# Kernel tuning notes

Hardware: AMD Instinct MI355X
Metric: run time of the kernel (lower is better)

The kernel has to match this reference:

```python
import jax, jax.numpy as jnp
import numpy as np

PAD_ID = 1
NEG = jnp.float32(-1e30)


def setup_inputs() -> dict:
    key = jax.random.key(0)
    ks = jax.random.split(key, 12)
    T, B, S, D, E, V = 20, 32, 400, 512, 512, 50000
    s = 0.02  # weight init scale for numerical sanity
    return {
        "inputs": jax.random.randint(ks[0], (T, B), 0, V),
        "src": jax.random.randint(ks[1], (S, B, 1), 0, V),
        "h_e": jax.random.normal(ks[2], (S, B, D), jnp.float32),
        "h0": jnp.zeros((B, D), jnp.float32),
        "c0": jnp.zeros((B, D), jnp.float32),
        "W_emb": jax.random.normal(ks[3], (V, E), jnp.float32) * s,
        "W_proj": jax.random.normal(ks[4], (E, 3 * D), jnp.float32) * s,
        "b_out": jax.random.normal(ks[5], (V,), jnp.float32) * s,
        "proj_u_W": jax.random.normal(ks[6], (1, 3 * D), jnp.float32) * s,
        "proj_u_b": jnp.zeros((1,), jnp.float32),
        "enc_W": jax.random.normal(ks[7], (D, D), jnp.float32) * s,
        "dec_W": jax.random.normal(ks[8], (D, D), jnp.float32) * s,
        "W_ih": jax.random.normal(ks[9], (4 * D, E), jnp.float32) * s,
        "W_hh": jax.random.normal(ks[10], (4 * D, D), jnp.float32) * s,
        "b_ih": jnp.zeros((4 * D,), jnp.float32),
        "b_hh": jnp.zeros((4 * D,), jnp.float32),
    }


def reference(inputs, src, h_e, h0, c0, W_emb, W_proj, b_out, proj_u_W,
              proj_u_b, enc_W, dec_W, W_ih, W_hh, b_ih, b_hh):
    T, B = inputs.shape
    D = h0.shape[1]
    V = W_emb.shape[0]
    src_bs = src[:, :, 0].T                       # [B, S]
    # Sect 2.4 shared output weights: W_out = tanh(W_emb @ W_proj)  [V, 3D]
    W_out = jnp.tanh(W_emb @ W_proj)
    rows = jnp.arange(B)[:, None]
    tpos = jnp.arange(T)

    def step(carry, xs):
        h, c, hist = carry                        # hist: [T, B, D] decoder-state history
        inp_t, t = xs
        emb = W_emb[inp_t]                        # [B, E]
        # single-layer LSTM cell (torch gate order i, f, g, o)
        gates = emb @ W_ih.T + h @ W_hh.T + b_ih + b_hh
        i, f, g, o = jnp.split(gates, 4, axis=-1)
        c_new = jax.nn.sigmoid(f) * c + jax.nn.sigmoid(i) * jnp.tanh(g)
        hd = jax.nn.sigmoid(o) * jnp.tanh(c_new)  # [B, D]
        # encoder intra-attention
        q = hd @ enc_W.T
        ae = jax.nn.softmax(jnp.einsum('bd,sbd->bs', q, h_e), axis=-1)  # [B, S]
        ce = jnp.einsum('bs,sbd->bd', ae, h_e)
        # decoder intra-attention over steps < t (zero context at t==0)
        qd = hd @ dec_W.T
        sd = jnp.einsum('bd,tbd->bt', qd, hist)
        sd = jnp.where(tpos[None, :] < t, sd, NEG)
        ad = jax.nn.softmax(sd, axis=-1)
        cd = jnp.where(t > 0, jnp.einsum('bt,tbd->bd', ad, hist), 0.0)
        hist = hist.at[t].set(hd)
        # pointer-generator
        ccat = jnp.concatenate([hd, ce, cd], axis=-1)        # [B, 3D]
        logits = ccat @ W_out.T + b_out                      # [B, V]
        logits = logits.at[:, PAD_ID].set(NEG)
        p_gen = jax.nn.softmax(logits, axis=-1)
        p_switch = jax.nn.sigmoid(ccat @ proj_u_W.T + proj_u_b)  # [B, 1]
        # copy distribution: scatter attention into vocab
        copy = jnp.zeros((B, V), logits.dtype).at[rows, src_bs].add(ae)
        scores = copy * p_switch + p_gen * (1.0 - p_switch)
        return (hd, c_new, hist), scores

    hist0 = jnp.zeros((T, B, D), h0.dtype)
    _, scores = jax.lax.scan(step, (h0, c0, hist0), (inputs, tpos))
    return scores  # [T, B, V]
```

## Files before the change

### kernel.cpp

```cpp
#include <hip/hip_runtime.h>
#include <stdint.h>

typedef unsigned short u16;
typedef unsigned int   u32;

using f32x4 = __attribute__((ext_vector_type(4))) float;
using s16x8 = __attribute__((ext_vector_type(8))) short;

#define TT 20
#define BB 32
#define SS 400
#define DD 512
#define VV 50000
#define VP 50048

__device__ __forceinline__ float bf2f(u16 u){
  u32 x = ((u32)u) << 16;
  return __builtin_bit_cast(float, x);
}
__device__ __forceinline__ u16 f2bf(float f){
  u32 x = __builtin_bit_cast(u32, f);
  x = x + 0x7fffu + ((x >> 16) & 1u);
  return (u16)(x >> 16);
}
__device__ __forceinline__ float sigm(float x){ return 1.0f/(1.0f + __expf(-x)); }
__device__ __forceinline__ float tanh_fast(float x){
  float a = fabsf(x);
  if (a < 0.25f){ float x2 = x*x; return x + x*x2*(-0.33333334f + 0.13333334f*x2); }
  return tanhf(x);
}
__device__ __forceinline__ void gld16(const void* g, void* l){
  __builtin_amdgcn_global_load_lds((const __attribute__((address_space(1))) void*)g,
                                   (__attribute__((address_space(3))) void*)l, 16, 0, 0);
}

__global__ __launch_bounds__(256) void k_prep(
    const float* __restrict__ W_proj,
    const float* __restrict__ W_ih,   const float* __restrict__ W_hh,
    const float* __restrict__ b_ih,   const float* __restrict__ b_hh,
    const float* __restrict__ h0,     const float* __restrict__ c0,
    const float* __restrict__ enc_W,  const float* __restrict__ dec_W,
    u16* __restrict__ WpT,
    u16* __restrict__ Wihs, u16* __restrict__ Whhs,
    u16* __restrict__ encWb, u16* __restrict__ decWb, float* __restrict__ bgs,
    float* __restrict__ hist, u16* __restrict__ histb, float* __restrict__ c_st,
    float* __restrict__ psE)
{
  int i = blockIdx.x*256 + threadIdx.x;
  if (i < 1280){ psE[i] = 0.0f; return; }
  i -= 1280;
  if (i < 2048){ int d = i >> 2, g = i & 3; bgs[i] = b_ih[g*512 + d] + b_hh[g*512 + d]; return; }
  i -= 2048;
  if (i < 16384){ float hv = h0[i]; hist[i] = hv; histb[i] = f2bf(hv); c_st[i] = c0[i]; return; }
  i -= 16384;
  if (i < 786432){ int j = i >> 9, k = i & 511; WpT[i] = f2bf(W_proj[k*1536 + j]); return; }
  i -= 786432;
  if (i < 1048576){
    int mp = i >> 9, k = i & 511; int d = mp >> 2, g = mp & 3;
    Wihs[i] = f2bf(W_ih[(size_t)(g*512 + d)*512 + k]); return; }
  i -= 1048576;
  if (i < 1048576){
    int mp = i >> 9, k = i & 511; int d = mp >> 2, g = mp & 3;
    Whhs[i] = f2bf(W_hh[(size_t)(g*512 + d)*512 + k]); return; }
  i -= 1048576;
  if (i < 262144){ encWb[i] = f2bf(enc_W[i]); return; }
  i -= 262144;
  if (i < 262144){ decWb[i] = f2bf(dec_W[i]); return; }
}

__global__ __launch_bounds__(256) void k_cast_emb(const float* __restrict__ in, u16* __restrict__ out){
  int i = blockIdx.x*256 + threadIdx.x;
  int base = i*4;
  if (base >= VP*DD) return;
  uint2 o;
  if (base < VV*DD){
    float4 v = *(const float4*)&in[base];
    o.x = (u32)f2bf(v.x) | ((u32)f2bf(v.y) << 16);
    o.y = (u32)f2bf(v.z) | ((u32)f2bf(v.w) << 16);
  } else { o.x = 0u; o.y = 0u; }
  *(uint2*)&out[base] = o;
}

__global__ __launch_bounds__(256) void k_cast_he(const float* __restrict__ in, u16* __restrict__ out){
  int i = blockIdx.x*256 + threadIdx.x;
  int base = i*4;
  if (base >= SS*BB*DD) return;
  const int s = base >> 14;
  const int b = (base >> 9) & 31;
  const int d = base & 511;
  float4 v = *(const float4*)&in[base];
  uint2 o;
  o.x = (u32)f2bf(v.x) | ((u32)f2bf(v.y) << 16);
  o.y = (u32)f2bf(v.z) | ((u32)f2bf(v.w) << 16);
  *(uint2*)&out[((size_t)(b*SS + s) << 9) + d] = o;
}

__global__ __launch_bounds__(256) void k_gather(const int* __restrict__ inp,
                                                const u16* __restrict__ Wb, u16* __restrict__ out){
  int i = blockIdx.x*256 + threadIdx.x;
  if (i >= TT*BB*DD) return;
  int r = i >> 9, k = i & 511;
  out[i] = Wb[(size_t)inp[r]*DD + k];
}

template<int EPI>
__device__ __forceinline__ void gemm_tile(
    const u16* __restrict__ A, const u16* __restrict__ B,
    float* __restrict__ Cf, u16* __restrict__ Cb, const float* __restrict__ bias,
    int K, int mt, int nt, int ldc, int nmax, char* smemc)
{
  u16* As = (u16*)smemc;
  u16* Bs = (u16*)(smemc + 8192);
  const int tid = threadIdx.x;
  const int w = tid >> 6, l = tid & 63;
  const int m0 = mt*128, n0 = nt*128;
  const int sgrow = l >> 2;
  const int sgk = (((l & 3) ^ ((l >> 3) & 3))) * 8;
  const int wm = (w >> 1)*64, wn = (w & 1)*64;
  const int fr = l & 15;
  const int fk = (((l >> 4) ^ ((l >> 1) & 3))) * 8;
  f32x4 acc[4][4] = {};
  for (int k0 = 0; k0 < K; k0 += 32){
    #pragma unroll
    for (int i = 0; i < 2; ++i){
      const int ci = w + i*4;
      gld16(A + (size_t)(m0 + ci*16 + sgrow)*K + (k0 + sgk), &As[ci*512]);
      gld16(B + (size_t)(n0 + ci*16 + sgrow)*K + (k0 + sgk), &Bs[ci*512]);
    }
    __syncthreads();
    s16x8 af[4], bfr[4];
    #pragma unroll
    for (int i = 0; i < 4; ++i){
      af[i]  = *(const s16x8*)&As[(wm + i*16 + fr)*32 + fk];
      bfr[i] = *(const s16x8*)&Bs[(wn + i*16 + fr)*32 + fk];
    }
    #pragma unroll
    for (int i = 0; i < 4; ++i)
      #pragma unroll
      for (int j = 0; j < 4; ++j)
        acc[i][j] = __builtin_amdgcn_mfma_f32_16x16x32_bf16(af[i], bfr[j], acc[i][j], 0, 0, 0);
    __syncthreads();
  }
  #pragma unroll
  for (int i = 0; i < 4; ++i){
    #pragma unroll
    for (int j = 0; j < 4; ++j){
      #pragma unroll
      for (int r = 0; r < 4; ++r){
        const int row = m0 + wm + i*16 + (l >> 4)*4 + r;
        const int col = n0 + wn + j*16 + fr;
        const float v = acc[i][j][r];
        if constexpr (EPI == 0){ Cf[(size_t)row*ldc + col] = v; }
        else if constexpr (EPI == 1){ Cb[(size_t)row*ldc + col] = f2bf(tanh_fast(v)); }
        else { if (col < nmax) Cb[(size_t)row*ldc + col] = f2bf(v + bias[col]); }
      }
    }
  }
}

template<int EPI, int ORD>
__global__ __launch_bounds__(256) void gemm_bt(
    const u16* __restrict__ A, const u16* __restrict__ B,
    float* __restrict__ Cf, u16* __restrict__ Cb, const float* __restrict__ bias,
    int K, int TM, int TN, int ldc, int nmax)
{
  __shared__ __align__(16) char smem[16384];
  int bid = blockIdx.x;
  if (ORD >= 1){
    const int n = TM*TN, x = bid & 7, i = bid >> 3;
    const int q = n >> 3, r = n & 7;
    bid = (x < r ? x*(q+1) : r*(q+1) + (x-r)*q) + i;
  }
  const int mt = (ORD == 1) ? bid / TN : bid % TM;
  const int nt = (ORD == 1) ? bid % TN : bid / TM;
  gemm_tile<EPI>(A, B, Cf, Cb, bias, K, mt, nt, ldc, nmax, smem);
}

__global__ __launch_bounds__(256) void k_lstm(
    const u16* __restrict__ Whhs, const float* __restrict__ X, const float* __restrict__ bgs,
    float* __restrict__ hist, u16* __restrict__ histb, float* __restrict__ c_st,
    u16* __restrict__ ccatb, int t)
{
  __shared__ __align__(16) u16 Hs[32*512];
  __shared__ __align__(16) u16 As[16*512];
  __shared__ float Cp[4][16][32];
  const int blk = blockIdx.x;
  const int tid = threadIdx.x;
  const int w = tid >> 6, l = tid & 63;
  const char* hsrc = (const char*)(histb + (size_t)t*16384);
  #pragma unroll
  for (int p = 0; p < 8; ++p)
    gld16(hsrc + p*4096 + w*1024 + l*16, (char*)Hs + p*4096 + w*1024);
  const char* asrc = (const char*)(Whhs + (size_t)blk*16*512);
  #pragma unroll
  for (int p = 0; p < 4; ++p)
    gld16(asrc + p*4096 + w*1024 + l*16, (char*)As + p*4096 + w*1024);
  __syncthreads();
  {
    const int fr = l & 15, fko = (l >> 4)*8;
    f32x4 acc0 = {}, acc1 = {};
    #pragma unroll
    for (int kk = 0; kk < 4; ++kk){
      const int kb = (w*4 + kk)*32;
      s16x8 af = *(const s16x8*)&As[fr*512 + kb + fko];
      s16x8 b0 = *(const s16x8*)&Hs[fr*512 + kb + fko];
      s16x8 b1 = *(const s16x8*)&Hs[(16 + fr)*512 + kb + fko];
      acc0 = __builtin_amdgcn_mfma_f32_16x16x32_bf16(af, b0, acc0, 0, 0, 0);
      acc1 = __builtin_amdgcn_mfma_f32_16x16x32_bf16(af, b1, acc1, 0, 0, 0);
    }
    #pragma unroll
    for (int r = 0; r < 4; ++r){
      Cp[w][(l >> 4)*4 + r][fr]      = acc0[r];
      Cp[w][(l >> 4)*4 + r][16 + fr] = acc1[r];
    }
  }
  __syncthreads();
  if (tid < 128){
    const int dl = tid >> 5, b = tid & 31;
    const int d = blk*4 + dl;
    const int bd = b*512 + d;
    float gv[4];
    #pragma unroll
    for (int g = 0; g < 4; ++g)
      gv[g] = Cp[0][dl*4 + g][b] + Cp[1][dl*4 + g][b] + Cp[2][dl*4 + g][b] + Cp[3][dl*4 + g][b];
    const float4 x4 = *(const float4*)&X[((size_t)(t*BB + b))*2048 + d*4];
    const float4 g4 = *(const float4*)&bgs[d*4];
    const float iv = gv[0] + x4.x + g4.x;
    const float fv = gv[1] + x4.y + g4.y;
    const float gg = gv[2] + x4.z + g4.z;
    const float ov = gv[3] + x4.w + g4.w;
    const float cn = sigm(fv)*c_st[bd] + sigm(iv)*tanhf(gg);
    const float hd = sigm(ov)*tanhf(cn);
    c_st[bd] = cn;
    hist[(size_t)(t + 1)*16384 + bd] = hd;
    const u16 hb = f2bf(hd);
    histb[(size_t)(t + 1)*16384 + bd] = hb;
    ccatb[((size_t)(t*BB + b))*1536 + d] = hb;
  }
}

__global__ __launch_bounds__(256) void k_bulkq(
    const u16* __restrict__ Hb, const u16* __restrict__ encWb, const u16* __restrict__ decWb,
    float* __restrict__ qe_all, float* __restrict__ qd_all)
{
  __shared__ __align__(16) char smem[16384];
  const int e = blockIdx.x;
  const int which = e / 20;
  const int e2 = e % 20;
  const int mt = e2 % 5, nt = e2 / 5;
  gemm_tile<0>(Hb, which ? decWb : encWb, which ? qd_all : qe_all,
               nullptr, nullptr, 512, mt, nt, 512, 0, smem);
}

__global__ __launch_bounds__(256) void k_attn(
    const u16* __restrict__ heb, const float* __restrict__ hist,
    const float* __restrict__ qe_all, const float* __restrict__ qd_all,
    const float* __restrict__ puW,
    u16* __restrict__ ccatb, float* __restrict__ aeall,
    float* __restrict__ psE, float* __restrict__ psD)
{
  __shared__ float hcur[512];
  __shared__ float qv[512];
  __shared__ float ael[SS];
  __shared__ float red[256];
  __shared__ float part[4*512];
  __shared__ float adl[TT];
  __shared__ float sdl[TT];
  __shared__ float shs[2];
  const int blk = blockIdx.x;
  const int tid = threadIdx.x;

  if (blk < 640){
    const int row = blk;
    const int t = row >> 5, b = row & 31;
    const float* hsrc = hist + (size_t)(t + 1)*16384 + b*512;
    const float* qsrc = qe_all + (size_t)row*512;
    hcur[tid] = hsrc[tid]; hcur[tid + 256] = hsrc[tid + 256];
    qv[tid] = qsrc[tid];   qv[tid + 256] = qsrc[tid + 256];
    __syncthreads();
    for (int pass = 0; pass < 7; ++pass){
      const int s = pass*64 + (tid >> 2);
      if (s < SS){
        const u16* gp = heb + ((size_t)(b*SS + s))*512 + (tid & 3)*128;
        const float* hp = qv + (tid & 3)*128;
        float p = 0.0f;
        #pragma unroll 4
        for (int k8 = 0; k8 < 128; k8 += 8){
          s16x8 g8 = *(const s16x8*)&gp[k8];
          #pragma unroll
          for (int q = 0; q < 8; ++q) p += bf2f((u16)g8[q])*hp[k8 + q];
        }
        p += __shfl_xor(p, 1); p += __shfl_xor(p, 2);
        if ((tid & 3) == 0) ael[s] = p;
      }
    }
    __syncthreads();
    float lm = -1e30f;
    for (int s = tid; s < SS; s += 256) lm = fmaxf(lm, ael[s]);
    red[tid] = lm; __syncthreads();
    for (int st = 128; st; st >>= 1){ if (tid < st) red[tid] = fmaxf(red[tid], red[tid + st]); __syncthreads(); }
    const float M = red[0]; __syncthreads();
    float ls = 0.0f;
    for (int s = tid; s < SS; s += 256){ float p = __expf(ael[s] - M); ael[s] = p; ls += p; }
    red[tid] = ls; __syncthreads();
    for (int st = 128; st; st >>= 1){ if (tid < st) red[tid] += red[tid + st]; __syncthreads(); }
    const float inv = 1.0f/red[0];
    __syncthreads();
    {
      const int g = tid >> 6, th = tid & 63;
      const int d0 = th*8;
      float a8[8] = {};
      for (int s = g; s < SS; s += 4){
        const float a = ael[s];
        s16x8 hv = *(const s16x8*)&heb[((size_t)(b*SS + s))*512 + d0];
        #pragma unroll
        for (int q = 0; q < 8; ++q) a8[q] += a*bf2f((u16)hv[q]);
      }
      *(float4*)&part[g*512 + d0]     = float4{a8[0], a8[1], a8[2], a8[3]};
      *(float4*)&part[g*512 + d0 + 4] = float4{a8[4], a8[5], a8[6], a8[7]};
    }
    __syncthreads();
    {
      const int dd = tid*2;
      float ce0 = part[dd]     + part[512 + dd]     + part[1024 + dd]     + part[1536 + dd];
      float ce1 = part[dd + 1] + part[512 + dd + 1] + part[1024 + dd + 1] + part[1536 + dd + 1];
      ce0 *= inv; ce1 *= inv;
      *(u32*)&ccatb[(size_t)row*1536 + 512 + dd] = (u32)f2bf(ce0) | ((u32)f2bf(ce1) << 16);
      float pv = hcur[dd]*puW[dd] + hcur[dd + 1]*puW[dd + 1]
               + ce0*puW[512 + dd] + ce1*puW[512 + dd + 1];
      red[tid] = pv;
    }
    __syncthreads();
    for (int st = 128; st; st >>= 1){ if (tid < st) red[tid] += red[tid + st]; __syncthreads(); }
    if (tid == 0) psE[row] = red[0];
    for (int s = tid; s < SS; s += 256) aeall[(size_t)row*SS + s] = ael[s]*inv;
  } else {
    const int row = blk - 640;
    const int t = row >> 5, b = row & 31;
    const float* qsrc = qd_all + (size_t)row*512;
    qv[tid] = qsrc[tid]; qv[tid + 256] = qsrc[tid + 256];
    __syncthreads();
    for (int u0 = 0; u0 < t; u0 += 8){
      const int u = u0 + (tid >> 5);
      if (u < t){
        const float* hu = hist + (size_t)(u + 1)*16384 + b*512;
        float p = 0.0f;
        #pragma unroll
        for (int j = 0; j < 4; ++j){
          const int kb = (tid & 31)*4 + j*128;
          const float4 h4 = *(const float4*)&hu[kb];
          const float4 q4 = *(const float4*)&qv[kb];
          p += h4.x*q4.x + h4.y*q4.y + h4.z*q4.z + h4.w*q4.w;
        }
        p += __shfl_xor(p, 1); p += __shfl_xor(p, 2); p += __shfl_xor(p, 4);
        p += __shfl_xor(p, 8); p += __shfl_xor(p, 16);
        if ((tid & 31) == 0) sdl[u] = p;
      }
    }
    __syncthreads();
    if (tid == 0 && t > 0){
      float m2 = -1e30f;
      for (int u = 0; u < t; ++u) m2 = fmaxf(m2, sdl[u]);
      float s2 = 0.0f;
      for (int u = 0; u < t; ++u){ float p = __expf(sdl[u] - m2); adl[u] = p; s2 += p; }
      shs[0] = 1.0f/s2;
    }
    __syncthreads();
    const float invd = (t > 0) ? shs[0] : 0.0f;
    const int d0 = tid*2;
    float e0 = 0.0f, e1 = 0.0f;
    for (int u = 0; u < t; ++u){
      const float a = adl[u];
      const float* hu = hist + (size_t)(u + 1)*16384 + b*512 + d0;
      e0 += a*hu[0]; e1 += a*hu[1];
    }
    e0 *= invd; e1 *= invd;
    *(u32*)&ccatb[(size_t)row*1536 + 1024 + d0] = (u32)f2bf(e0) | ((u32)f2bf(e1) << 16);
    float pv = e0*puW[1024 + d0] + e1*puW[1024 + d0 + 1];
    red[tid] = pv; __syncthreads();
    for (int st = 128; st; st >>= 1){ if (tid < st) red[tid] += red[tid + st]; __syncthreads(); }
    if (tid == 0) psD[row] = red[0];
  }
}

__global__ __launch_bounds__(256) void k_softmax(
    const u16* __restrict__ lg, float* __restrict__ out,
    const float* __restrict__ psE, const float* __restrict__ psD, const float* __restrict__ puB)
{
  const int r = blockIdx.x, tid = threadIdx.x;
  __shared__ float rm[256], rs[256];
  const u16* row = lg + (size_t)r*VP;
  float m = -1e30f, s = 0.0f;
  for (int v8 = tid*8; v8 < VV; v8 += 2048){
    uint4 pk = *(const uint4*)&row[v8];
    u32 wds[4] = {pk.x, pk.y, pk.z, pk.w};
    #pragma unroll
    for (int q = 0; q < 8; ++q){
      if (v8 + q == 1) continue;
      float x = bf2f((u16)((wds[q >> 1] >> ((q & 1)*16)) & 0xffffu));
      if (x > m){ s = s*__expf(m - x) + 1.0f; m = x; }
      else s += __expf(x - m);
    }
  }
  rm[tid] = m; rs[tid] = s; __syncthreads();
  for (int st = 128; st; st >>= 1){
    if (tid < st){
      float m2 = fmaxf(rm[tid], rm[tid + st]);
      rs[tid] = rs[tid]*__expf(rm[tid] - m2) + rs[tid + st]*__expf(rm[tid + st] - m2);
      rm[tid] = m2;
    }
    __syncthreads();
  }
  const float M = rm[0];
  const float ps = 1.0f/(1.0f + __expf(-(psE[r] + psD[r] + puB[0])));
  const float inv = (1.0f - ps)/rs[0];
  float* orow = out + (size_t)r*VV;
  for (int v8 = tid*8; v8 < VV; v8 += 2048){
    uint4 pk = *(const uint4*)&row[v8];
    u32 wds[4] = {pk.x, pk.y, pk.z, pk.w};
    float o[8];
    #pragma unroll
    for (int q = 0; q < 8; ++q){
      float x = bf2f((u16)((wds[q >> 1] >> ((q & 1)*16)) & 0xffffu));
      o[q] = (v8 + q == 1) ? 0.0f : __expf(x - M)*inv;
    }
    *(float4*)&orow[v8]     = float4{o[0], o[1], o[2], o[3]};
    *(float4*)&orow[v8 + 4] = float4{o[4], o[5], o[6], o[7]};
  }
}

__global__ __launch_bounds__(256) void k_scatter(
    float* __restrict__ out, const int* __restrict__ src,
    const float* __restrict__ ae_all,
    const float* __restrict__ psE, const float* __restrict__ psD, const float* __restrict__ puB)
{
  const int idx = blockIdx.x*256 + threadIdx.x;
  if (idx >= TT*BB*SS) return;
  const int s = idx % SS;
  const int rb = idx / SS;
  const int b = rb & 31;
  const int v = src[s*BB + b];
  const float ps = 1.0f/(1.0f + __expf(-(psE[rb] + psD[rb] + puB[0])));
  atomicAdd(&out[(size_t)rb*VV + v], ae_all[(size_t)rb*SS + s]*ps);
}

extern "C" void kernel_launch(void* const* d_in, const int* in_sizes, int n_in,
                              void* d_out, int out_size, void* d_ws, size_t ws_size,
                              hipStream_t stream)
{
  const int*   inputs = (const int*)  d_in[0];
  const int*   src    = (const int*)  d_in[1];
  const float* h_e    = (const float*)d_in[2];
  const float* h0     = (const float*)d_in[3];
  const float* c0     = (const float*)d_in[4];
  const float* W_emb  = (const float*)d_in[5];
  const float* W_proj = (const float*)d_in[6];
  const float* b_out  = (const float*)d_in[7];
  const float* puW    = (const float*)d_in[8];
  const float* puB    = (const float*)d_in[9];
  const float* enc_W  = (const float*)d_in[10];
  const float* dec_W  = (const float*)d_in[11];
  const float* W_ih   = (const float*)d_in[12];
  const float* W_hh   = (const float*)d_in[13];
  const float* b_ih   = (const float*)d_in[14];
  const float* b_hh   = (const float*)d_in[15];
  float* out = (float*)d_out;

  char* wp = (char*)d_ws;
  auto alloc = [&](size_t bytes) -> char* {
    char* p = wp; wp += (bytes + 255) & ~(size_t)255; return p;
  };
  u16*   Wembb = (u16*)  alloc((size_t)VP*DD*2);
  u16*   WpT   = (u16*)  alloc(1536*512*2);
  u16*   heb   = (u16*)  alloc((size_t)SS*BB*DD*2);
  u16*   logitsb = (u16*)Wembb;
  u16*   Woutb = (u16*)  alloc((size_t)VP*1536*2);
  u16*   Wihs  = (u16*)  alloc(2048*512*2);
  u16*   Whhs  = (u16*)  alloc(2048*512*2);
  u16*   encWb = (u16*)  alloc(512*512*2);
  u16*   decWb = (u16*)  alloc(512*512*2);
  float* bgs   = (float*)alloc(2048*4);
  u16*   emba  = (u16*)  alloc((size_t)TT*BB*DD*2);
  float* X     = (float*)alloc((size_t)TT*BB*2048*4);
  float* c_st  = (float*)alloc(BB*DD*4);
  float* hist  = (float*)alloc((size_t)(TT+1)*BB*DD*4);
  u16*   histb = (u16*)  alloc((size_t)(TT+1)*BB*DD*2);
  u16*   ccatb = (u16*)  alloc((size_t)TT*BB*1536*2);
  float* aeall = (float*)alloc((size_t)TT*BB*SS*4);
  float* psE   = (float*)alloc(1280*4);
  float* psD   = psE + 640;
  float* qe_all= (float*)alloc((size_t)TT*BB*DD*4);
  float* qd_all= (float*)alloc((size_t)TT*BB*DD*4);

  k_prep<<<13389, 256, 0, stream>>>(W_proj, W_ih, W_hh, b_ih, b_hh, h0, c0, enc_W, dec_W,
                                    WpT, Wihs, Whhs, encWb, decWb, bgs, hist, histb, c_st, psE);
  k_cast_emb<<<(VP*DD/4)/256, 256, 0, stream>>>(W_emb, Wembb);
  k_cast_he<<<(SS*BB*DD/4)/256, 256, 0, stream>>>(h_e, heb);
  k_gather<<<(TT*BB*DD + 255)/256, 256, 0, stream>>>(inputs, Wembb, emba);

  gemm_bt<0,0><<<5*16,   256, 0, stream>>>(emba, Wihs, X, nullptr, nullptr, 512, 5, 16, 2048, 0);
  gemm_bt<1,1><<<391*12, 256, 0, stream>>>(Wembb, WpT, nullptr, Woutb, nullptr, 512, 391, 12, 1536, 0);

  for (int t = 0; t < TT; ++t)
    k_lstm<<<128, 256, 0, stream>>>(Whhs, X, bgs, hist, histb, c_st, ccatb, t);

  k_bulkq<<<40, 256, 0, stream>>>(histb + 16384, encWb, decWb, qe_all, qd_all);
  k_attn<<<1280, 256, 0, stream>>>(heb, hist, qe_all, qd_all, puW, ccatb, aeall, psE, psD);

  gemm_bt<3,2><<<5*391, 256, 0, stream>>>(ccatb, Woutb, nullptr, logitsb, b_out, 1536, 5, 391, VP, VV);
  k_softmax<<<TT*BB, 256, 0, stream>>>(logitsb, out, psE, psD, puB);
  k_scatter<<<(TT*BB*SS + 255)/256, 256, 0, stream>>>(out, src, aeall, psE, psD, puB);
}
```

Baseline: 547.4 us.

## Use 256x256-tile triple-buffered bf16 MFMA GEMM for output weight and logits

Adds a new 512-thread GEMM kernel with 256x256 output tiles, a swizzled LDS layout, a triple-buffered global-to-LDS prefetch pipeline and split MFMA phases with priority hints. It replaces the older GEMM for both the tanh(W_emb@W_proj) product and the final logits GEMM. Vocabulary padding grows to a multiple of 256 and the ccat buffer is padded to 768 rows so the large tiles divide evenly. The aim is more data reuse per tile and less global traffic, at the cost of higher register and LDS use (lower occupancy) and extra padded work, especially in M for the logits GEMM.

```diff
diff --git a/kernel.cpp b/kernel.cpp
--- a/kernel.cpp
+++ b/kernel.cpp
@@ -12,7 +12,7 @@
 #define SS 400
 #define DD 512
 #define VV 50000
-#define VP 50048
+#define VP2 50176
 
 __device__ __forceinline__ float bf2f(u16 u){
   u32 x = ((u32)u) << 16;
@@ -71,7 +71,7 @@
 __global__ __launch_bounds__(256) void k_cast_emb(const float* __restrict__ in, u16* __restrict__ out){
   int i = blockIdx.x*256 + threadIdx.x;
   int base = i*4;
-  if (base >= VP*DD) return;
+  if (base >= VP2*DD) return;
   uint2 o;
   if (base < VV*DD){
     float4 v = *(const float4*)&in[base];
@@ -174,6 +174,121 @@
   const int mt = (ORD == 1) ? bid / TN : bid % TM;
   const int nt = (ORD == 1) ? bid % TN : bid / TM;
   gemm_tile<EPI>(A, B, Cf, Cb, bias, K, mt, nt, ldc, nmax, smem);
+}
+
+template<int EPI, int ORD>
+__global__ __launch_bounds__(512, 2) void gemm256(
+    const u16* __restrict__ A, const u16* __restrict__ B,
+    u16* __restrict__ Cb, const float* __restrict__ bias,
+    int K, int TM, int TN, int ldc, int mmax, int nmax)
+{
+  __shared__ __align__(16) u16 ldsm[49152];
+  const int tid = threadIdx.x;
+  const int w = tid >> 6, l = tid & 63;
+  int bid = blockIdx.x;
+  { const int n = TM*TN, x = bid & 7, i2 = bid >> 3;
+    const int q = n >> 3, r = n & 7;
+    bid = (x < r ? x*(q+1) : r*(q+1) + (x-r)*q) + i2; }
+  const int mt = (ORD == 1) ? bid / TN : bid % TM;
+  const int nt = (ORD == 1) ? bid % TN : bid / TM;
+  const int m0 = mt*256, n0 = nt*256;
+  const int NK = K >> 5;
+
+  const u32 lin  = (u32)tid << 4;
+  const u32 srow = lin >> 6;
+  const u32 scbh = ((lin & 63) ^ ((((lin >> 7) ^ (lin >> 9)) & 3u) << 4)) >> 1;
+  const u16* gA0 = A + (size_t)(m0 + (int)srow)*K + scbh;
+  const u16* gA1 = A + (size_t)(m0 + 128 + (int)srow)*K + scbh;
+  const u16* gB0 = B + (size_t)(n0 + (int)srow)*K + scbh;
+  const u16* gB1 = B + (size_t)(n0 + 128 + (int)srow)*K + scbh;
+  char* const lds8 = (char*)ldsm;
+  const int woff = w << 10;
+
+  const int gcol = (l >> 4) << 4;
+  int offA[8], offB[4];
+  #pragma unroll
+  for (int fm = 0; fm < 8; ++fm){
+    const int row = ((w >> 2) << 7) + fm*16 + (l & 15);
+    const int byt = (row & 127)*64 + gcol;
+    offA[fm] = (row >> 7)*8192 + (byt ^ ((((byt >> 7) ^ (byt >> 9)) & 3) << 4));
+  }
+  #pragma unroll
+  for (int fn = 0; fn < 4; ++fn){
+    const int row = ((w & 3) << 6) + fn*16 + (l & 15);
+    const int byt = (row & 127)*64 + gcol;
+    offB[fn] = 16384 + (row >> 7)*8192 + (byt ^ ((((byt >> 7) ^ (byt >> 9)) & 3) << 4));
+  }
+
+  f32x4 acc[8][4] = {};
+
+  {
+    char* d0 = lds8 + woff;
+    gld16(gA0, d0); gld16(gA1, d0 + 8192); gld16(gB0, d0 + 16384); gld16(gB1, d0 + 24576);
+    char* d1 = lds8 + 32768 + woff;
+    gld16(gA0 + 32, d1); gld16(gA1 + 32, d1 + 8192);
+    gld16(gB0 + 32, d1 + 16384); gld16(gB1 + 32, d1 + 24576);
+  }
+  asm volatile("s_waitcnt vmcnt(4)" ::: "memory");
+  __builtin_amdgcn_s_barrier();
+
+  int bufc = 0, bufs = 65536;
+  for (int T = 0; T < NK; ++T){
+    s16x8 af[4], bf[4], af2[4];
+    #pragma unroll
+    for (int fm = 0; fm < 4; ++fm) af[fm] = *(const s16x8*)(lds8 + bufc + offA[fm]);
+    #pragma unroll
+    for (int fn = 0; fn < 4; ++fn) bf[fn] = *(const s16x8*)(lds8 + bufc + offB[fn]);
+    {
+      const size_t ko = (size_t)((T + 2 < NK) ? (T + 2) : 0) * 32;
+      char* d = lds8 + bufs + woff;
+      gld16(gA0 + ko, d); gld16(gA1 + ko, d + 8192);
+      gld16(gB0 + ko, d + 16384); gld16(gB1 + ko, d + 24576);
+    }
+    __builtin_amdgcn_s_barrier();
+    asm volatile("s_waitcnt lgkmcnt(0)" ::: "memory");
+    __builtin_amdgcn_sched_barrier(0);
+    __builtin_amdgcn_s_setprio(1);
+    #pragma unroll
+    for (int fm = 0; fm < 4; ++fm)
+      #pragma unroll
+      for (int fn = 0; fn < 4; ++fn)
+        acc[fm][fn] = __builtin_amdgcn_mfma_f32_16x16x32_bf16(af[fm], bf[fn], acc[fm][fn], 0, 0, 0);
+    __builtin_amdgcn_s_setprio(0);
+    #pragma unroll
+    for (int fm = 0; fm < 4; ++fm) af2[fm] = *(const s16x8*)(lds8 + bufc + offA[fm + 4]);
+    asm volatile("s_waitcnt lgkmcnt(0)" ::: "memory");
+    __builtin_amdgcn_sched_barrier(0);
+    __builtin_amdgcn_s_setprio(1);
+    #pragma unroll
+    for (int fm = 0; fm < 4; ++fm)
+      #pragma unroll
+      for (int fn = 0; fn < 4; ++fn)
+        acc[fm + 4][fn] = __builtin_amdgcn_mfma_f32_16x16x32_bf16(af2[fm], bf[fn], acc[fm + 4][fn], 0, 0, 0);
+    __builtin_amdgcn_s_setprio(0);
+    asm volatile("s_waitcnt vmcnt(4)" ::: "memory");
+    __builtin_amdgcn_s_barrier();
+    bufc = (bufc == 65536) ? 0 : bufc + 32768;
+    bufs = (bufs == 65536) ? 0 : bufs + 32768;
+  }
+
+  #pragma unroll
+  for (int fm = 0; fm < 8; ++fm){
+    #pragma unroll
+    for (int fn = 0; fn < 4; ++fn){
+      #pragma unroll
+      for (int rr = 0; rr < 4; ++rr){
+        const int row = m0 + ((w >> 2) << 7) + fm*16 + ((l >> 4) << 2) + rr;
+        const int col = n0 + ((w & 3) << 6) + fn*16 + (l & 15);
+        const float v = acc[fm][fn][rr];
+        if constexpr (EPI == 1){
+          Cb[(size_t)row*ldc + col] = f2bf(tanh_fast(v));
+        } else {
+          if (row < mmax && col < nmax)
+            Cb[(size_t)row*ldc + col] = f2bf(v + bias[col]);
+        }
+      }
+    }
+  }
 }
 
 __global__ __launch_bounds__(256) void k_lstm(
@@ -389,7 +504,7 @@
 {
   const int r = blockIdx.x, tid = threadIdx.x;
   __shared__ float rm[256], rs[256];
-  const u16* row = lg + (size_t)r*VP;
+  const u16* row = lg + (size_t)r*VP2;
   float m = -1e30f, s = 0.0f;
   for (int v8 = tid*8; v8 < VV; v8 += 2048){
     uint4 pk = *(const uint4*)&row[v8];
@@ -470,11 +585,11 @@
   auto alloc = [&](size_t bytes) -> char* {
     char* p = wp; wp += (bytes + 255) & ~(size_t)255; return p;
   };
-  u16*   Wembb = (u16*)  alloc((size_t)VP*DD*2);
+  u16*   Wembb = (u16*)  alloc((size_t)VP2*DD*2);
   u16*   WpT   = (u16*)  alloc(1536*512*2);
   u16*   heb   = (u16*)  alloc((size_t)SS*BB*DD*2);
   u16*   logitsb = (u16*)Wembb;
-  u16*   Woutb = (u16*)  alloc((size_t)VP*1536*2);
+  u16*   Woutb = (u16*)  alloc((size_t)VP2*1536*2);
   u16*   Wihs  = (u16*)  alloc(2048*512*2);
   u16*   Whhs  = (u16*)  alloc(2048*512*2);
   u16*   encWb = (u16*)  alloc(512*512*2);
@@ -485,7 +600,7 @@
   float* c_st  = (float*)alloc(BB*DD*4);
   float* hist  = (float*)alloc((size_t)(TT+1)*BB*DD*4);
   u16*   histb = (u16*)  alloc((size_t)(TT+1)*BB*DD*2);
-  u16*   ccatb = (u16*)  alloc((size_t)TT*BB*1536*2);
+  u16*   ccatb = (u16*)  alloc((size_t)768*1536*2);
   float* aeall = (float*)alloc((size_t)TT*BB*SS*4);
   float* psE   = (float*)alloc(1280*4);
   float* psD   = psE + 640;
@@ -494,12 +609,13 @@
 
   k_prep<<<13389, 256, 0, stream>>>(W_proj, W_ih, W_hh, b_ih, b_hh, h0, c0, enc_W, dec_W,
                                     WpT, Wihs, Whhs, encWb, decWb, bgs, hist, histb, c_st, psE);
-  k_cast_emb<<<(VP*DD/4)/256, 256, 0, stream>>>(W_emb, Wembb);
+  k_cast_emb<<<(VP2*DD/4)/256, 256, 0, stream>>>(W_emb, Wembb);
   k_cast_he<<<(SS*BB*DD/4)/256, 256, 0, stream>>>(h_e, heb);
   k_gather<<<(TT*BB*DD + 255)/256, 256, 0, stream>>>(inputs, Wembb, emba);
 
-  gemm_bt<0,0><<<5*16,   256, 0, stream>>>(emba, Wihs, X, nullptr, nullptr, 512, 5, 16, 2048, 0);
-  gemm_bt<1,1><<<391*12, 256, 0, stream>>>(Wembb, WpT, nullptr, Woutb, nullptr, 512, 391, 12, 1536, 0);
+  gemm_bt<0,0><<<5*16, 256, 0, stream>>>(emba, Wihs, X, nullptr, nullptr, 512, 5, 16, 2048, 0);
+
+  gemm256<1,1><<<196*6, 512, 0, stream>>>(Wembb, WpT, Woutb, nullptr, 512, 196, 6, 1536, 0, 0);
 
   for (int t = 0; t < TT; ++t)
     k_lstm<<<128, 256, 0, stream>>>(Whhs, X, bgs, hist, histb, c_st, ccatb, t);
@@ -507,7 +623,8 @@
   k_bulkq<<<40, 256, 0, stream>>>(histb + 16384, encWb, decWb, qe_all, qd_all);
   k_attn<<<1280, 256, 0, stream>>>(heb, hist, qe_all, qd_all, puW, ccatb, aeall, psE, psD);
 
-  gemm_bt<3,2><<<5*391, 256, 0, stream>>>(ccatb, Woutb, nullptr, logitsb, b_out, 1536, 5, 391, VP, VV);
+  gemm256<3,2><<<3*196, 512, 0, stream>>>(ccatb, Woutb, logitsb, b_out, 1536, 3, 196, VP2, 640, VV);
+
   k_softmax<<<TT*BB, 256, 0, stream>>>(logitsb, out, psE, psD, puB);
   k_scatter<<<(TT*BB*SS + 255)/256, 256, 0, stream>>>(out, src, aeall, psE, psD, puB);
 }
```

New measurement: 610.7 us. +11.6%, slower.

## Double GEMM K-step to 64 with XOR-swizzled LDS and fold scatter into softmax

Applied to the files above, without the earlier changes.

The shared bf16 GEMM tile now loads 64 K-elements per stage into a 32KB XOR-swizzled LDS buffer, halving the number of barrier pairs per K loop. The vocab padding grows to 50176 so the tile grid covers it, and grid sizes are updated to match. The copy-distribution scatter is folded into the tail of the softmax kernel, which removes one launch and rereads of psE/psD. The larger LDS footprint may lower occupancy in the GEMM kernels.

```diff
diff --git a/kernel.cpp b/kernel.cpp
--- a/kernel.cpp
+++ b/kernel.cpp
@@ -12,7 +12,7 @@
 #define SS 400
 #define DD 512
 #define VV 50000
-#define VP 50048
+#define VP2 50176
 
 __device__ __forceinline__ float bf2f(u16 u){
   u32 x = ((u32)u) << 16;
@@ -71,7 +71,7 @@
 __global__ __launch_bounds__(256) void k_cast_emb(const float* __restrict__ in, u16* __restrict__ out){
   int i = blockIdx.x*256 + threadIdx.x;
   int base = i*4;
-  if (base >= VP*DD) return;
+  if (base >= VP2*DD) return;
   uint2 o;
   if (base < VV*DD){
     float4 v = *(const float4*)&in[base];
@@ -110,35 +110,39 @@
     int K, int mt, int nt, int ldc, int nmax, char* smemc)
 {
   u16* As = (u16*)smemc;
-  u16* Bs = (u16*)(smemc + 8192);
+  u16* Bs = (u16*)(smemc + 16384);
   const int tid = threadIdx.x;
   const int w = tid >> 6, l = tid & 63;
   const int m0 = mt*128, n0 = nt*128;
-  const int sgrow = l >> 2;
-  const int sgk = (((l & 3) ^ ((l >> 3) & 3))) * 8;
+  const int srow = tid >> 3;
+  const int scol = ((tid & 7) ^ ((tid >> 3) & 7)) * 8;
   const int wm = (w >> 1)*64, wn = (w & 1)*64;
   const int fr = l & 15;
-  const int fk = (((l >> 4) ^ ((l >> 1) & 3))) * 8;
+  const int g4 = l >> 4;
   f32x4 acc[4][4] = {};
-  for (int k0 = 0; k0 < K; k0 += 32){
-    #pragma unroll
-    for (int i = 0; i < 2; ++i){
-      const int ci = w + i*4;
-      gld16(A + (size_t)(m0 + ci*16 + sgrow)*K + (k0 + sgk), &As[ci*512]);
-      gld16(B + (size_t)(n0 + ci*16 + sgrow)*K + (k0 + sgk), &Bs[ci*512]);
-    }
-    __syncthreads();
-    s16x8 af[4], bfr[4];
-    #pragma unroll
-    for (int i = 0; i < 4; ++i){
-      af[i]  = *(const s16x8*)&As[(wm + i*16 + fr)*32 + fk];
-      bfr[i] = *(const s16x8*)&Bs[(wn + i*16 + fr)*32 + fk];
-    }
-    #pragma unroll
-    for (int i = 0; i < 4; ++i)
+  for (int k0 = 0; k0 < K; k0 += 64){
+    #pragma unroll
+    for (int j = 0; j < 4; ++j){
+      gld16(A + (size_t)(m0 + j*32 + srow)*K + k0 + scol, (char*)As + j*4096 + (w << 10));
+      gld16(B + (size_t)(n0 + j*32 + srow)*K + k0 + scol, (char*)Bs + j*4096 + (w << 10));
+    }
+    __syncthreads();
+    #pragma unroll
+    for (int h = 0; h < 2; ++h){
+      s16x8 af[4], bfr[4];
       #pragma unroll
-      for (int j = 0; j < 4; ++j)
-        acc[i][j] = __builtin_amdgcn_mfma_f32_16x16x32_bf16(af[i], bfr[j], acc[i][j], 0, 0, 0);
+      for (int i = 0; i < 4; ++i){
+        const int ra = wm + i*16 + fr;
+        af[i]  = *(const s16x8*)((char*)As + ra*128 + ((((h << 2) + g4) ^ (ra & 7)) << 4));
+        const int rb = wn + i*16 + fr;
+        bfr[i] = *(const s16x8*)((char*)Bs + rb*128 + ((((h << 2) + g4) ^ (rb & 7)) << 4));
+      }
+      #pragma unroll
+      for (int i = 0; i < 4; ++i)
+        #pragma unroll
+        for (int j2 = 0; j2 < 4; ++j2)
+          acc[i][j2] = __builtin_amdgcn_mfma_f32_16x16x32_bf16(af[i], bfr[j2], acc[i][j2], 0, 0, 0);
+    }
     __syncthreads();
   }
   #pragma unroll
@@ -164,7 +168,7 @@
     float* __restrict__ Cf, u16* __restrict__ Cb, const float* __restrict__ bias,
     int K, int TM, int TN, int ldc, int nmax)
 {
-  __shared__ __align__(16) char smem[16384];
+  __shared__ __align__(16) char smem[32768];
   int bid = blockIdx.x;
   if (ORD >= 1){
     const int n = TM*TN, x = bid & 7, i = bid >> 3;
@@ -243,7 +247,7 @@
     const u16* __restrict__ Hb, const u16* __restrict__ encWb, const u16* __restrict__ decWb,
     float* __restrict__ qe_all, float* __restrict__ qd_all)
 {
-  __shared__ __align__(16) char smem[16384];
+  __shared__ __align__(16) char smem[32768];
   const int e = blockIdx.x;
   const int which = e / 20;
   const int e2 = e % 20;
@@ -385,11 +389,12 @@
 
 __global__ __launch_bounds__(256) void k_softmax(
     const u16* __restrict__ lg, float* __restrict__ out,
-    const float* __restrict__ psE, const float* __restrict__ psD, const float* __restrict__ puB)
+    const float* __restrict__ psE, const float* __restrict__ psD, const float* __restrict__ puB,
+    const int* __restrict__ src, const float* __restrict__ ae_all)
 {
   const int r = blockIdx.x, tid = threadIdx.x;
   __shared__ float rm[256], rs[256];
-  const u16* row = lg + (size_t)r*VP;
+  const u16* row = lg + (size_t)r*VP2;
   float m = -1e30f, s = 0.0f;
   for (int v8 = tid*8; v8 < VV; v8 += 2048){
     uint4 pk = *(const uint4*)&row[v8];
@@ -427,21 +432,12 @@
     *(float4*)&orow[v8]     = float4{o[0], o[1], o[2], o[3]};
     *(float4*)&orow[v8 + 4] = float4{o[4], o[5], o[6], o[7]};
   }
-}
-
-__global__ __launch_bounds__(256) void k_scatter(
-    float* __restrict__ out, const int* __restrict__ src,
-    const float* __restrict__ ae_all,
-    const float* __restrict__ psE, const float* __restrict__ psD, const float* __restrict__ puB)
-{
-  const int idx = blockIdx.x*256 + threadIdx.x;
-  if (idx >= TT*BB*SS) return;
-  const int s = idx % SS;
-  const int rb = idx / SS;
-  const int b = rb & 31;
-  const int v = src[s*BB + b];
-  const float ps = 1.0f/(1.0f + __expf(-(psE[rb] + psD[rb] + puB[0])));
-  atomicAdd(&out[(size_t)rb*VV + v], ae_all[(size_t)rb*SS + s]*ps);
+  __syncthreads();
+  const int b = r & 31;
+  for (int sp = tid; sp < SS; sp += 256){
+    const int v = src[sp*BB + b];
+    atomicAdd(&orow[v], ae_all[(size_t)r*SS + sp]*ps);
+  }
 }
 
 extern "C" void kernel_launch(void* const* d_in, const int* in_sizes, int n_in,
@@ -470,11 +466,11 @@
   auto alloc = [&](size_t bytes) -> char* {
     char* p = wp; wp += (bytes + 255) & ~(size_t)255; return p;
   };
-  u16*   Wembb = (u16*)  alloc((size_t)VP*DD*2);
+  u16*   Wembb = (u16*)  alloc((size_t)VP2*DD*2);
   u16*   WpT   = (u16*)  alloc(1536*512*2);
   u16*   heb   = (u16*)  alloc((size_t)SS*BB*DD*2);
   u16*   logitsb = (u16*)Wembb;
-  u16*   Woutb = (u16*)  alloc((size_t)VP*1536*2);
+  u16*   Woutb = (u16*)  alloc((size_t)VP2*1536*2);
   u16*   Wihs  = (u16*)  alloc(2048*512*2);
   u16*   Whhs  = (u16*)  alloc(2048*512*2);
   u16*   encWb = (u16*)  alloc(512*512*2);
@@ -494,12 +490,13 @@
 
   k_prep<<<13389, 256, 0, stream>>>(W_proj, W_ih, W_hh, b_ih, b_hh, h0, c0, enc_W, dec_W,
                                     WpT, Wihs, Whhs, encWb, decWb, bgs, hist, histb, c_st, psE);
-  k_cast_emb<<<(VP*DD/4)/256, 256, 0, stream>>>(W_emb, Wembb);
+  k_cast_emb<<<(VP2*DD/4)/256, 256, 0, stream>>>(W_emb, Wembb);
   k_cast_he<<<(SS*BB*DD/4)/256, 256, 0, stream>>>(h_e, heb);
   k_gather<<<(TT*BB*DD + 255)/256, 256, 0, stream>>>(inputs, Wembb, emba);
 
-  gemm_bt<0,0><<<5*16,   256, 0, stream>>>(emba, Wihs, X, nullptr, nullptr, 512, 5, 16, 2048, 0);
-  gemm_bt<1,1><<<391*12, 256, 0, stream>>>(Wembb, WpT, nullptr, Woutb, nullptr, 512, 391, 12, 1536, 0);
+  gemm_bt<0,0><<<5*16, 256, 0, stream>>>(emba, Wihs, X, nullptr, nullptr, 512, 5, 16, 2048, 0);
+
+  gemm_bt<1,1><<<392*12, 256, 0, stream>>>(Wembb, WpT, nullptr, Woutb, nullptr, 512, 392, 12, 1536, 0);
 
   for (int t = 0; t < TT; ++t)
     k_lstm<<<128, 256, 0, stream>>>(Whhs, X, bgs, hist, histb, c_st, ccatb, t);
@@ -507,7 +504,7 @@
   k_bulkq<<<40, 256, 0, stream>>>(histb + 16384, encWb, decWb, qe_all, qd_all);
   k_attn<<<1280, 256, 0, stream>>>(heb, hist, qe_all, qd_all, puW, ccatb, aeall, psE, psD);
 
-  gemm_bt<3,2><<<5*391, 256, 0, stream>>>(ccatb, Woutb, nullptr, logitsb, b_out, 1536, 5, 391, VP, VV);
-  k_softmax<<<TT*BB, 256, 0, stream>>>(logitsb, out, psE, psD, puB);
-  k_scatter<<<(TT*BB*SS + 255)/256, 256, 0, stream>>>(out, src, aeall, psE, psD, puB);
-}
+  gemm_bt<3,2><<<5*392, 256, 0, stream>>>(ccatb, Woutb, nullptr, logitsb, b_out, 1536, 5, 392, VP2, VV);
+
+  k_softmax<<<TT*BB, 256, 0, stream>>>(logitsb, out, psE, psD, puB, src, aeall);
+}
```

New measurement: 508.3 us. 1.08x faster.
